# Kernel tuning notes

Measured on AMD Instinct MI355X. Metric: run time of the kernel, lower is better.

Reference implementation:

```python
import jax, jax.numpy as jnp
import numpy as np

KH = KW = 3  # kernel spatial size is hard-coded to 3 in the original layer


def _tdiv2(x):
    # matches tf.cast(x / 2, tf.int32): true-divide by 2, truncate toward zero
    return jnp.trunc(x * 0.5)


def setup_inputs() -> dict:
    key = jax.random.key(0)
    k1, k2, k3 = jax.random.split(key, 3)
    B, H, W, C, F = 4, 32, 32, 64, 128
    # integer-valued tensors stored as float32 (bit-serial math needs integer weights)
    inputs = jax.random.randint(k1, (B, H, W, C), 0, 16).astype(jnp.float32)
    kernel = jax.random.randint(k2, (KH, KW, C, F), -8, 8).astype(jnp.float32)
    bias = jax.random.randint(k3, (F,), -4, 4).astype(jnp.float32)
    return {"inputs": inputs, "kernel": kernel, "bias": bias, "bits": 4}


def reference(inputs, kernel, bias, bits):
    # Bit-serial conv2d, padding='same' (pad=1), activation='relu'.
    # Per (kernel position, input element, output channel) the original computes
    #   acc <- trunc((acc + x * (w mod 2) * sign(w_orig)) / 2); w <- trunc(w / 2)
    # for `bits` iterations, then sums over channels/kernel window.
    B, H, W, C = inputs.shape
    F = kernel.shape[-1]
    x = jnp.pad(inputs, ((0, 0), (1, 1), (1, 1), (0, 0)))  # 'same' padding, pad=1
    out = jnp.zeros((B, H, W, F), inputs.dtype)
    for i in range(KH):
        for j in range(KW):
            patch = x[:, i:i + H, j:j + W, :][..., None]   # [B,H,W,C,1]
            w = kernel[i, j]                               # [C,F]
            s = jnp.sign(w)                                # sign of ORIGINAL weight, fixed
            acc = jnp.zeros((B, H, W, C, F), inputs.dtype)
            ww = w
            for _ in range(bits):
                acc = _tdiv2(acc + patch * (jnp.mod(ww, 2.0) * s))
                ww = _tdiv2(ww)
            out = out + acc.sum(axis=3)                    # sum over C; kernel window summed by loop
    return jax.nn.relu(out + bias)
```

## Files before the change

### kernel.cpp

```cpp
#include <hip/hip_runtime.h>
#include <stdint.h>


typedef short s16x2 __attribute__((ext_vector_type(2)));

#define NWPK 36864

__global__ __launch_bounds__(256) void prep_w(const float* __restrict__ kern,
                                              uint32_t* __restrict__ ws) {
    int t  = blockIdx.x * 256 + threadIdx.x;
    int u  = t & 3;
    int f  = (t >> 2) & 127;
    int cq = (t >> 9) & 3;
    int gk = t >> 11;
    int g  = gk & 1;
    int ki = gk >> 1;
    int c  = cq * 16 + g * 8 + u * 2;
    int wlo = (int)kern[(ki * 64 + c    ) * 128 + f];
    int whi = (int)kern[(ki * 64 + c + 1) * 128 + f];
    ws[t] = (uint32_t)(uint16_t)(int16_t)wlo |
            ((uint32_t)(uint16_t)(int16_t)whi << 16);
}

__global__ __launch_bounds__(512, 4) void conv_main(const uint32_t* __restrict__ ws,
                                                    const float* __restrict__ input,
                                                    const float* __restrict__ bias,
                                                    float* __restrict__ out) {
    int bid = blockIdx.x;
    int wq  = bid & 3;
    int h   = (bid >> 2) & 31;
    int b   = bid >> 7;
    int tid = threadIdx.x;
    int f   = tid & 127;
    int cq  = tid >> 7;
    int w0  = wq * 8;

    __shared__ uint32_t xl[3 * 10 * 32];
    __shared__ int prt[4 * 8 * 128];

    if (tid < 480) {
        int q   = tid & 15;
        int rc  = tid >> 4;
        int col = rc % 10;
        int r   = rc / 10;
        int hp  = h + r - 1;
        int wp  = w0 + col - 1;
        int2 v2 = {0, 0};
        if (hp >= 0 && hp < 32 && wp >= 0 && wp < 32) {
            const float4 v = *(const float4*)&input[(((b * 32) + hp) * 32 + wp) * 64 + q * 4];
            v2.x = (int)v.x | ((int)v.y << 16);
            v2.y = (int)v.z | ((int)v.w << 16);
        }
        *(int2*)&xl[rc * 32 + q * 2] = v2;
    }

    const int4* wp4 = (const int4*)ws;
    int bv = (int)bias[f];

    __syncthreads();

    s16x2 acc[8];
    #pragma unroll
    for (int i = 0; i < 8; ++i) acc[i] = (s16x2){0, 0};

    #pragma unroll
    for (int ki = 0; ki < 9; ++ki) {
        const int row = ki / 3, jj = ki % 3;
        #pragma unroll
        for (int g = 0; g < 2; ++g) {
            const int4 w4 = wp4[(ki * 2 + g) * 512 + tid];
            const uint32_t* xrow = xl + (row * 10 + jj) * 32 + cq * 8 + g * 4;
            #pragma unroll
            for (int half = 0; half < 2; ++half) {
                int4 xv[4];
                #pragma unroll
                for (int p = 0; p < 4; ++p)
                    xv[p] = *(const int4*)(xrow + (half * 4 + p) * 32);
                #pragma unroll
                for (int u = 0; u < 4; ++u) {
                    s16x2 w2 = __builtin_bit_cast(s16x2, (&w4.x)[u]);
                    s16x2 A  = (w2 >> 15) & (short)15;
                    #pragma unroll
                    for (int p = 0; p < 4; ++p) {
                        s16x2 xs = __builtin_bit_cast(s16x2, (&xv[p].x)[u]);
                        acc[half * 4 + p] += (xs * w2 + A) >> 4;
                    }
                }
            }
        }
    }

    #pragma unroll
    for (int px = 0; px < 8; ++px) {
        int a = __builtin_bit_cast(int, acc[px]);
        prt[(cq * 8 + px) * 128 + f] = (int)(short)(a & 0xffff) + (a >> 16);
    }
    __syncthreads();

    #pragma unroll
    for (int k = 0; k < 2; ++k) {
        int px = (tid >> 7) + k * 4;
        int v = prt[(0 * 8 + px) * 128 + f] + prt[(1 * 8 + px) * 128 + f] +
                prt[(2 * 8 + px) * 128 + f] + prt[(3 * 8 + px) * 128 + f] + bv;
        out[((b * 32 + h) * 32 + w0 + px) * 128 + f] = (float)(v < 0 ? 0 : v);
    }
}

extern "C" void kernel_launch(void* const* d_in, const int* in_sizes, int n_in,
                              void* d_out, int out_size, void* d_ws, size_t ws_size,
                              hipStream_t stream) {
    const float* input  = (const float*)d_in[0];
    const float* kernel = (const float*)d_in[1];
    const float* bias   = (const float*)d_in[2];

    uint32_t* ws = (uint32_t*)d_ws;

    prep_w<<<144, 256, 0, stream>>>(kernel, ws);
    conv_main<<<512, 512, 0, stream>>>(ws, input, bias, (float*)d_out);
}
```

Measured before the change: 76.83 us.

## Fuse weight packing into conv kernel and reuse input row across kernel columns

Drops the separate weight-prep launch. The conv kernel now reads float weights straight from the original kernel tensor and packs them to int16 pairs in registers. The inner loop now loads one padded input row of 10 columns into registers and reuses it for all three kernel columns, which cuts LDS reads. The cost is more scalar global float loads per thread, which are strided and only coalesced across f, plus extra conversion work and register pressure that could hurt occupancy.

New measurement: 78.52 us. 2.2% more time.

```diff
diff --git a/kernel.cpp b/kernel.cpp
--- a/kernel.cpp
+++ b/kernel.cpp
@@ -4,28 +4,10 @@
 
 typedef short s16x2 __attribute__((ext_vector_type(2)));
 
-#define NWPK 36864
-
-__global__ __launch_bounds__(256) void prep_w(const float* __restrict__ kern,
-                                              uint32_t* __restrict__ ws) {
-    int t  = blockIdx.x * 256 + threadIdx.x;
-    int u  = t & 3;
-    int f  = (t >> 2) & 127;
-    int cq = (t >> 9) & 3;
-    int gk = t >> 11;
-    int g  = gk & 1;
-    int ki = gk >> 1;
-    int c  = cq * 16 + g * 8 + u * 2;
-    int wlo = (int)kern[(ki * 64 + c    ) * 128 + f];
-    int whi = (int)kern[(ki * 64 + c + 1) * 128 + f];
-    ws[t] = (uint32_t)(uint16_t)(int16_t)wlo |
-            ((uint32_t)(uint16_t)(int16_t)whi << 16);
-}
-
-__global__ __launch_bounds__(512, 4) void conv_main(const uint32_t* __restrict__ ws,
-                                                    const float* __restrict__ input,
-                                                    const float* __restrict__ bias,
-                                                    float* __restrict__ out) {
+__global__ __launch_bounds__(512, 4) void conv_fused(const float* __restrict__ kern,
+                                                     const float* __restrict__ input,
+                                                     const float* __restrict__ bias,
+                                                     float* __restrict__ out) {
     int bid = blockIdx.x;
     int wq  = bid & 3;
     int h   = (bid >> 2) & 31;
@@ -54,8 +36,8 @@
         *(int2*)&xl[rc * 32 + q * 2] = v2;
     }
 
-    const int4* wp4 = (const int4*)ws;
     int bv = (int)bias[f];
+    const float* wbase = kern + (cq * 16) * 128 + f;
 
     __syncthreads();
 
@@ -64,26 +46,34 @@
     for (int i = 0; i < 8; ++i) acc[i] = (s16x2){0, 0};
 
     #pragma unroll
-    for (int ki = 0; ki < 9; ++ki) {
-        const int row = ki / 3, jj = ki % 3;
+    for (int r = 0; r < 3; ++r) {
         #pragma unroll
         for (int g = 0; g < 2; ++g) {
-            const int4 w4 = wp4[(ki * 2 + g) * 512 + tid];
-            const uint32_t* xrow = xl + (row * 10 + jj) * 32 + cq * 8 + g * 4;
+            int4 xv[10];
+            const uint32_t* xrow = xl + r * 10 * 32 + cq * 8 + g * 4;
             #pragma unroll
-            for (int half = 0; half < 2; ++half) {
-                int4 xv[4];
-                #pragma unroll
-                for (int p = 0; p < 4; ++p)
-                    xv[p] = *(const int4*)(xrow + (half * 4 + p) * 32);
+            for (int col = 0; col < 10; ++col)
+                xv[col] = *(const int4*)(xrow + col * 32);
+            #pragma unroll
+            for (int jj = 0; jj < 3; ++jj) {
+                int ki = r * 3 + jj;
+                s16x2 wv[4], Av[4];
                 #pragma unroll
                 for (int u = 0; u < 4; ++u) {
-                    s16x2 w2 = __builtin_bit_cast(s16x2, (&w4.x)[u]);
-                    s16x2 A  = (w2 >> 15) & (short)15;
+                    int c = g * 8 + u * 2;
+                    int wlo = (int)wbase[(ki * 64 + c    ) * 128];
+                    int whi = (int)wbase[(ki * 64 + c + 1) * 128];
+                    uint32_t wpk = (uint32_t)(uint16_t)(int16_t)wlo |
+                                   ((uint32_t)(uint16_t)(int16_t)whi << 16);
+                    wv[u] = __builtin_bit_cast(s16x2, wpk);
+                    Av[u] = (wv[u] >> 15) & (short)15;
+                }
+                #pragma unroll
+                for (int u = 0; u < 4; ++u) {
                     #pragma unroll
-                    for (int p = 0; p < 4; ++p) {
-                        s16x2 xs = __builtin_bit_cast(s16x2, (&xv[p].x)[u]);
-                        acc[half * 4 + p] += (xs * w2 + A) >> 4;
+                    for (int px = 0; px < 8; ++px) {
+                        s16x2 xs = __builtin_bit_cast(s16x2, (&xv[jj + px].x)[u]);
+                        acc[px] += (xs * wv[u] + Av[u]) >> 4;
                     }
                 }
             }
@@ -113,8 +103,5 @@
     const float* kernel = (const float*)d_in[1];
     const float* bias   = (const float*)d_in[2];
 
-    uint32_t* ws = (uint32_t*)d_ws;
-
-    prep_w<<<144, 256, 0, stream>>>(kernel, ws);
-    conv_main<<<512, 512, 0, stream>>>(ws, input, bias, (float*)d_out);
+    conv_fused<<<512, 512, 0, stream>>>(kernel, input, bias, (float*)d_out);
 }
```
